# Performance work log

Hardware: AMD Instinct MI355X
Metric: run time of the kernel (lower is better)

The kernel has to match this reference:

```python
import jax, jax.numpy as jnp
import numpy as np

D_MODEL = 1024
N_HEADS = 16
D_HEAD = D_MODEL // N_HEADS


def _pid_proj(x, Wp, Wi, Wd, Wg, bg):
    # x: (B, T, D). PID decomposition: proportional / integral (running mean) / derivative (diff).
    T = x.shape[1]
    denom = jnp.arange(1, T + 1, dtype=x.dtype)[None, :, None]
    integral = jnp.cumsum(x, axis=1) / denom
    derivative = jnp.concatenate([jnp.zeros_like(x[:, :1]), x[:, 1:] - x[:, :-1]], axis=1)
    g = jax.nn.softmax(x @ Wg.T + bg, axis=-1)  # (B, T, 3)
    return (g[..., 0:1] * (x @ Wp.T)
            + g[..., 1:2] * (integral @ Wi.T)
            + g[..., 2:3] * (derivative @ Wd.T))


def setup_inputs() -> dict:
    key = jax.random.key(0)
    ks = jax.random.split(key, 16)
    B, T, D = 2, 2048, D_MODEL
    s = 1.0 / np.sqrt(D)

    def lin(k):
        return jax.random.uniform(k, (D, D), jnp.float32, -s, s)

    inp = {"x": jax.random.normal(ks[0], (B, T, D), jnp.float32)}
    names = ["q", "k", "v"]
    i = 1
    for n in names:
        inp[n + "Wp"] = lin(ks[i]); i += 1
        inp[n + "Wi"] = lin(ks[i]) * 0.1; i += 1
        inp[n + "Wd"] = lin(ks[i]) * 0.1; i += 1
        inp[n + "Wg"] = jax.random.uniform(ks[i], (3, D), jnp.float32, -s, s); i += 1
        inp[n + "bg"] = jnp.array([1.0, 0.0, 0.0], jnp.float32)
    inp["oW"] = lin(ks[i]); i += 1
    inp["ob"] = jax.random.uniform(ks[i], (D,), jnp.float32, -s, s)
    return inp


def reference(x, qWp, qWi, qWd, qWg, qbg,
              kWp, kWi, kWd, kWg, kbg,
              vWp, vWi, vWd, vWg, vbg, oW, ob):
    B, T, D = x.shape
    H, dh = N_HEADS, D_HEAD
    Q = _pid_proj(x, qWp, qWi, qWd, qWg, qbg).reshape(B, T, H, dh).transpose(0, 2, 1, 3)
    K = _pid_proj(x, kWp, kWi, kWd, kWg, kbg).reshape(B, T, H, dh).transpose(0, 2, 1, 3)
    V = _pid_proj(x, vWp, vWi, vWd, vWg, vbg).reshape(B, T, H, dh).transpose(0, 2, 1, 3)
    scale = jnp.sqrt(jnp.asarray(dh, x.dtype))
    scores = jnp.einsum('bhqd,bhkd->bhqk', Q, K) / scale  # (B,H,T,T)
    causal = jnp.triu(jnp.ones((T, T), bool), k=1)
    scores = jnp.where(causal[None, None], -jnp.inf, scores)
    attn = jax.nn.softmax(scores, axis=-1)
    out = jnp.einsum('bhqk,bhkd->bhqd', attn, V)
    out = out.transpose(0, 2, 1, 3).reshape(B, T, D)
    return out @ oW.T + ob
```

## Files before the change

### kernel.cpp

```cpp
#include <hip/hip_runtime.h>
#include <hip/hip_bf16.h>


#define D_MODEL 1024
#define T_SEQ   2048
#define B_SZ    2
#define M_ROWS  (B_SZ * T_SEQ)
#define N_HEADS 16
#define D_HEAD  64

typedef unsigned short u16;
typedef unsigned int   u32;

typedef short  short8  __attribute__((ext_vector_type(8)));
typedef float  float4v __attribute__((ext_vector_type(4)));

__device__ __forceinline__ float bf2f(u16 u) {
    union { u32 i; float f; } c; c.i = ((u32)u) << 16; return c.f;
}
__device__ __forceinline__ u16 f2bf(float f) {
    union { float f; u32 i; } c; c.f = f;
    u32 i = c.i;
    i += 0x7FFFu + ((i >> 16) & 1u);
    return (u16)(i >> 16);
}
__device__ __forceinline__ u16 f2bfc(float f) {
    __hip_bfloat16 h = __float2bfloat16(f);
    union { __hip_bfloat16 h; u16 u; } c; c.h = h; return c.u;
}
__device__ __forceinline__ float ldin(const void* p, int i, int fl) {
    return fl ? ((const float*)p)[i] : bf2f(((const u16*)p)[i]);
}

__global__ void detect_kernel(const u32* __restrict__ x, int* __restrict__ flag)
{
    if (threadIdx.x == 0 && blockIdx.x == 0) {
        int good = 0;
        for (int i = 0; i < 256; ++i) {
            union { u32 u; float f; } c; c.u = x[i];
            float a = fabsf(c.f);
            if (c.f == c.f && a > 1e-8f && a < 1e4f) ++good;
        }
        *flag = (good >= 192) ? 1 : 0;
    }
}

__global__ __launch_bounds__(256) void scan_partial(
    const void* __restrict__ x, float* __restrict__ csum,
    const int* __restrict__ flagp)
{
    int fl = *flagp;
    int tid = blockIdx.x * 256 + threadIdx.x;
    int b = tid >> 14;
    int c = (tid >> 10) & 15;
    int d = tid & 1023;
    int base = (b * T_SEQ + c * 128) * D_MODEL + d;
    float s = 0.f;
#pragma unroll 8
    for (int t = 0; t < 128; ++t) s += ldin(x, base + t * D_MODEL, fl);
    csum[tid] = s;
}

__global__ __launch_bounds__(256) void scan_final(
    const void* __restrict__ x, const float* __restrict__ csum,
    u16* __restrict__ integ, const int* __restrict__ flagp)
{
    int fl = *flagp;
    int tid = blockIdx.x * 256 + threadIdx.x;
    int b = tid >> 14;
    int c = (tid >> 10) & 15;
    int d = tid & 1023;
    float pre = 0.f;
    int cbase = (b << 14) | d;
    for (int cc = 0; cc < c; ++cc) pre += csum[cbase + (cc << 10)];
    int base = (b * T_SEQ + c * 128) * D_MODEL + d;
    float run = pre;
    int t0 = c * 128;
    for (int t = 0; t < 128; ++t) {
        run += ldin(x, base + t * D_MODEL, fl);
        integ[base + t * D_MODEL] = f2bf(run / (float)(t0 + t + 1));
    }
}

__global__ __launch_bounds__(64) void gates_kernel(
    const void* __restrict__ x,
    const void* __restrict__ qWg, const void* __restrict__ qbg,
    const void* __restrict__ kWg, const void* __restrict__ kbg,
    const void* __restrict__ vWg, const void* __restrict__ vbg,
    float* __restrict__ gq, float* __restrict__ gk, float* __restrict__ gv,
    const int* __restrict__ flagp)
{
    int fl = *flagp;
    int row = blockIdx.x;
    int l = threadIdx.x;
    int xb = row * D_MODEL;
    float p[9];
#pragma unroll
    for (int j = 0; j < 9; ++j) p[j] = 0.f;
#pragma unroll 4
    for (int i = 0; i < 16; ++i) {
        int d = l + 64 * i;
        float xv = ldin(x, xb + d, fl);
        p[0] += xv * ldin(qWg, d, fl);
        p[1] += xv * ldin(qWg, 1024 + d, fl);
        p[2] += xv * ldin(qWg, 2048 + d, fl);
        p[3] += xv * ldin(kWg, d, fl);
        p[4] += xv * ldin(kWg, 1024 + d, fl);
        p[5] += xv * ldin(kWg, 2048 + d, fl);
        p[6] += xv * ldin(vWg, d, fl);
        p[7] += xv * ldin(vWg, 1024 + d, fl);
        p[8] += xv * ldin(vWg, 2048 + d, fl);
    }
#pragma unroll
    for (int off = 32; off > 0; off >>= 1) {
#pragma unroll
        for (int j = 0; j < 9; ++j) p[j] += __shfl_down(p[j], off);
    }
    if (l == 0) {
        const void* bgs[3] = { qbg, kbg, vbg };
        float* outs[3] = { gq, gk, gv };
#pragma unroll
        for (int pr = 0; pr < 3; ++pr) {
            float a0 = p[pr * 3 + 0] + ldin(bgs[pr], 0, fl);
            float a1 = p[pr * 3 + 1] + ldin(bgs[pr], 1, fl);
            float a2 = p[pr * 3 + 2] + ldin(bgs[pr], 2, fl);
            float mx = fmaxf(a0, fmaxf(a1, a2));
            float e0 = __expf(a0 - mx), e1 = __expf(a1 - mx), e2 = __expf(a2 - mx);
            float inv = 1.f / (e0 + e1 + e2);
            outs[pr][row * 3 + 0] = e0 * inv;
            outs[pr][row * 3 + 1] = e1 * inv;
            outs[pr][row * 3 + 2] = e2 * inv;
        }
    }
}

struct CvtArgs { const void* src[10]; };

__global__ __launch_bounds__(256) void cvt_w(
    CvtArgs a, u16* __restrict__ dst, const int* __restrict__ flagp)
{
    int fl = *flagp;
    int m = blockIdx.y;
    u16* d = dst + ((size_t)m << 20);
    int i = (blockIdx.x * 256 + threadIdx.x) * 8;
    if (fl) {
        const float* s = (const float*)a.src[m];
        float4 v0 = *(const float4*)(s + i);
        float4 v1 = *(const float4*)(s + i + 4);
        ushort4 o0, o1;
        o0.x = f2bfc(v0.x); o0.y = f2bfc(v0.y); o0.z = f2bfc(v0.z); o0.w = f2bfc(v0.w);
        o1.x = f2bfc(v1.x); o1.y = f2bfc(v1.y); o1.z = f2bfc(v1.z); o1.w = f2bfc(v1.w);
        *(ushort4*)(d + i) = o0;
        *(ushort4*)(d + i + 4) = o1;
    } else {
        const u16* s = (const u16*)a.src[m];
        *(ushort4*)(d + i)     = *(const ushort4*)(s + i);
        *(ushort4*)(d + i + 4) = *(const ushort4*)(s + i + 4);
    }
}

struct GemmArgs {
    const void* W[3][3];
    const float* G[3];
    u16* C[3];
};

template<int MODE, int BW16>
__global__ __launch_bounds__(256, 3) void mfma_gemm(
    const void* __restrict__ X, const u16* __restrict__ Ib,
    const u16* __restrict__ Abf, GemmArgs args,
    const void* __restrict__ bias, void* __restrict__ outp,
    const int* __restrict__ flagp, int Ktot)
{
    int fl = *flagp;
    __shared__ __align__(16) u16 As[2 * 4096];
    __shared__ __align__(16) u16 Bs[2 * 4096];

    int tid = threadIdx.x;
    int l = tid & 63, w = tid >> 6;
    int wm = w >> 1, wn = w & 1;
    int m0 = blockIdx.y * 128, n0 = blockIdx.x * 128;
    int z = blockIdx.z;
    int lane15 = l & 15, quad = l >> 4;
    int srow = tid >> 2;
    int cs = tid & 3;
    int skof = cs * 8;

    const void* W0; const void* W1; const void* W2;
    const float* G = nullptr;
    u16* Chead = nullptr;
    if (MODE == 0) {
        W0 = args.W[z][0]; W1 = args.W[z][1]; W2 = args.W[z][2];
        G = args.G[z]; Chead = args.C[z];
    } else {
        W0 = args.W[0][0]; W1 = W0; W2 = W0;
    }

    float gcoef[2][3];
    if (MODE == 0) {
#pragma unroll
        for (int c = 0; c < 2; ++c)
#pragma unroll
            for (int s = 0; s < 3; ++s)
                gcoef[c][s] = G[(m0 + c * 64 + srow) * 3 + s];
    }

    ushort4 ra[2][4];
    ushort4 rb[2][2];

    auto cvt4 = [](float4 t) {
        ushort4 u;
        u.x = f2bf(t.x); u.y = f2bf(t.y); u.z = f2bf(t.z); u.w = f2bf(t.w);
        return u;
    };
    auto ld8 = [&](const void* p, int idx, ushort4& o0, ushort4& o1) {
        if (fl) {
            o0 = cvt4(*(const float4*)((const float*)p + idx));
            o1 = cvt4(*(const float4*)((const float*)p + idx + 4));
        } else {
            o0 = *(const ushort4*)((const u16*)p + idx);
            o1 = *(const ushort4*)((const u16*)p + idx + 4);
        }
    };

    auto load_phase = [&](int k0) {
        int seg = k0 >> 10, ksrc = k0 & 1023;
        const void* Wse = (MODE == 0) ? (seg == 0 ? W0 : (seg == 1 ? W1 : W2)) : W0;
#pragma unroll
        for (int c = 0; c < 2; ++c) {
            int gm = m0 + c * 64 + srow;
            int idx = gm * 1024 + ksrc + skof;
            if (MODE == 1) {
                ra[c][0] = *(const ushort4*)&Abf[idx];
                ra[c][1] = *(const ushort4*)&Abf[idx + 4];
            } else if (seg == 1) {
                ra[c][0] = *(const ushort4*)&Ib[idx];
                ra[c][1] = *(const ushort4*)&Ib[idx + 4];
            } else {
                ld8(X, idx, ra[c][0], ra[c][1]);
                if (seg == 2 && (gm & (T_SEQ - 1)) != 0)
                    ld8(X, idx - 1024, ra[c][2], ra[c][3]);
            }
            int gn = n0 + c * 64 + srow;
            int bidx = gn * 1024 + ksrc + skof;
            if (BW16) {
                const u16* bs = (const u16*)Wse;
                rb[c][0] = *(const ushort4*)&bs[bidx];
                rb[c][1] = *(const ushort4*)&bs[bidx + 4];
            } else {
                ld8(Wse, bidx, rb[c][0], rb[c][1]);
            }
        }
    };

    auto unp8 = [](ushort4 a, ushort4 b, float v[8]) {
        v[0] = bf2f(a.x); v[1] = bf2f(a.y); v[2] = bf2f(a.z); v[3] = bf2f(a.w);
        v[4] = bf2f(b.x); v[5] = bf2f(b.y); v[6] = bf2f(b.z); v[7] = bf2f(b.w);
    };

    int wo[2];
#pragma unroll
    for (int c = 0; c < 2; ++c) {
        int g = c * 16 + ((srow >> 4) << 2) + cs;
        wo[c] = (g << 7) | ((((srow & 15) + g) & 15) << 3);
    }

    auto store_phase = [&](int k0, int buf) {
        int seg = k0 >> 10;
        u16* Ad = As + buf * 4096;
        u16* Bd = Bs + buf * 4096;
#pragma unroll
        for (int c = 0; c < 2; ++c) {
            int row = c * 64 + srow;
            short8 pk;
            if (MODE == 1) {
                pk[0] = (short)ra[c][0].x; pk[1] = (short)ra[c][0].y;
                pk[2] = (short)ra[c][0].z; pk[3] = (short)ra[c][0].w;
                pk[4] = (short)ra[c][1].x; pk[5] = (short)ra[c][1].y;
                pk[6] = (short)ra[c][1].z; pk[7] = (short)ra[c][1].w;
            } else {
                float v[8];
                unp8(ra[c][0], ra[c][1], v);
                if (seg == 2) {
                    int gm = m0 + row;
                    if ((gm & (T_SEQ - 1)) == 0) {
#pragma unroll
                        for (int j = 0; j < 8; ++j) v[j] = 0.f;
                    } else {
                        float pv[8];
                        unp8(ra[c][2], ra[c][3], pv);
#pragma unroll
                        for (int j = 0; j < 8; ++j) v[j] -= pv[j];
                    }
                }
                float sc = gcoef[c][seg];
#pragma unroll
                for (int j = 0; j < 8; ++j) pk[j] = (short)f2bfc(v[j] * sc);
            }
            *(short8*)&Ad[wo[c]] = pk;

            short8 pb;
            pb[0] = (short)rb[c][0].x; pb[1] = (short)rb[c][0].y;
            pb[2] = (short)rb[c][0].z; pb[3] = (short)rb[c][0].w;
            pb[4] = (short)rb[c][1].x; pb[5] = (short)rb[c][1].y;
            pb[6] = (short)rb[c][1].z; pb[7] = (short)rb[c][1].w;
            *(short8*)&Bd[wo[c]] = pb;
        }
    };

    float4v acc[4][4];
#pragma unroll
    for (int i = 0; i < 4; ++i)
#pragma unroll
        for (int j = 0; j < 4; ++j)
#pragma unroll
            for (int r = 0; r < 4; ++r) acc[i][j][r] = 0.f;

    int aro[4], bro[4];
#pragma unroll
    for (int t = 0; t < 4; ++t) {
        int ga = (wm * 4 + t) * 4 + quad;
        aro[t] = (ga << 7) | (((lane15 + ga) & 15) << 3);
        int gb = (wn * 4 + t) * 4 + quad;
        bro[t] = (gb << 7) | (((lane15 + gb) & 15) << 3);
    }

    int nIt = Ktot >> 5;
    load_phase(0);
    store_phase(0, 0);

    for (int it = 0; it < nIt; ++it) {
        __syncthreads();
        int cur = it & 1;
        if (it + 1 < nIt) load_phase((it + 1) << 5);

        short8 af[4], bfr[4];
#pragma unroll
        for (int ms = 0; ms < 4; ++ms)
            af[ms] = *(const short8*)&As[cur * 4096 + aro[ms]];
#pragma unroll
        for (int ns = 0; ns < 4; ++ns)
            bfr[ns] = *(const short8*)&Bs[cur * 4096 + bro[ns]];
#pragma unroll
        for (int ms = 0; ms < 4; ++ms)
#pragma unroll
            for (int ns = 0; ns < 4; ++ns)
                acc[ms][ns] = __builtin_amdgcn_mfma_f32_16x16x32_bf16(
                    af[ms], bfr[ns], acc[ms][ns], 0, 0, 0);

        if (it + 1 < nIt) store_phase((it + 1) << 5, 1 - cur);
    }

#pragma unroll
    for (int ms = 0; ms < 4; ++ms) {
#pragma unroll
        for (int r = 0; r < 4; ++r) {
            int m = m0 + wm * 64 + ms * 16 + quad * 4 + r;
#pragma unroll
            for (int ns = 0; ns < 4; ++ns) {
                int n = n0 + wn * 64 + ns * 16 + lane15;
                float vv = acc[ms][ns][r];
                if (MODE == 0) {
                    int b = m >> 11, t = m & (T_SEQ - 1);
                    int h = n >> 6,  d = n & 63;
                    Chead[(((b << 4) + h) * T_SEQ + t) * 64 + d] = f2bf(vv);
                } else {
                    vv += ldin(bias, n, fl);
                    if (fl) ((float*)outp)[m * 1024 + n] = vv;
                    else    ((u16*)outp)[m * 1024 + n] = f2bf(vv);
                }
            }
        }
    }
}

__global__ __launch_bounds__(256) void attn_mfma(
    const u16* __restrict__ Qh, const u16* __restrict__ Kh,
    const u16* __restrict__ Vh, u16* __restrict__ AO)
{
    int bx = blockIdx.x;
    int qt = bx & 31;
    int bh = bx >> 5;
    int h  = bh & 15;
    int b  = bh >> 4;
    int tid = threadIdx.x;
    int l   = tid & 63;
    int w   = tid >> 6;
    int lane15 = l & 15;
    int quad   = l >> 4;

    __shared__ __align__(16) u16 Ks[64 * 72];
    __shared__ __align__(16) u16 Vt[64 * 72];
    __shared__ __align__(16) u16 Ps[4 * 16 * 72];

    const u16* Qb = Qh + bh * (T_SEQ * 64);
    const u16* Kb = Kh + bh * (T_SEQ * 64);
    const u16* Vb = Vh + bh * (T_SEQ * 64);

    int qrow = qt * 64 + w * 16 + lane15;
    short8 qf[2];
#pragma unroll
    for (int ks = 0; ks < 2; ++ks)
        qf[ks] = *(const short8*)&Qb[qrow * 64 + ks * 32 + quad * 8];

    float4v oacc[4];
#pragma unroll
    for (int ds = 0; ds < 4; ++ds)
#pragma unroll
        for (int r = 0; r < 4; ++r) oacc[ds][r] = 0.f;
    float mrun[4], lrun[4];
#pragma unroll
    for (int r = 0; r < 4; ++r) { mrun[r] = -1e30f; lrun[r] = 0.f; }

    int srow = tid >> 2;
    int sdc  = (tid & 3) * 16;

    for (int kt = 0; kt <= qt; ++kt) {
        {
            const u16* kp = &Kb[(kt * 64 + srow) * 64 + sdc];
            ushort4 a = *(const ushort4*)kp;
            ushort4 c = *(const ushort4*)(kp + 4);
            ushort4 d2 = *(const ushort4*)(kp + 8);
            ushort4 e = *(const ushort4*)(kp + 12);
            short8 p0, p1;
            p0[0]=a.x; p0[1]=a.y; p0[2]=a.z; p0[3]=a.w;
            p0[4]=c.x; p0[5]=c.y; p0[6]=c.z; p0[7]=c.w;
            p1[0]=d2.x; p1[1]=d2.y; p1[2]=d2.z; p1[3]=d2.w;
            p1[4]=e.x; p1[5]=e.y; p1[6]=e.z; p1[7]=e.w;
            *(short8*)&Ks[srow * 72 + sdc] = p0;
            *(short8*)&Ks[srow * 72 + sdc + 8] = p1;

            const u16* vp = &Vb[(kt * 64 + srow) * 64 + sdc];
            u16 vv[16];
            *(ushort4*)&vv[0]  = *(const ushort4*)vp;
            *(ushort4*)&vv[4]  = *(const ushort4*)(vp + 4);
            *(ushort4*)&vv[8]  = *(const ushort4*)(vp + 8);
            *(ushort4*)&vv[12] = *(const ushort4*)(vp + 12);
#pragma unroll
            for (int e2 = 0; e2 < 16; ++e2)
                Vt[(sdc + e2) * 72 + srow] = vv[e2];
        }
        __syncthreads();

        float4v sacc[4];
#pragma unroll
        for (int ns = 0; ns < 4; ++ns)
#pragma unroll
            for (int r = 0; r < 4; ++r) sacc[ns][r] = 0.f;
#pragma unroll
        for (int ks = 0; ks < 2; ++ks) {
#pragma unroll
            for (int ns = 0; ns < 4; ++ns) {
                short8 bfk = *(const short8*)&Ks[(ns * 16 + lane15) * 72 + ks * 32 + quad * 8];
                sacc[ns] = __builtin_amdgcn_mfma_f32_16x16x32_bf16(
                    qf[ks], bfk, sacc[ns], 0, 0, 0);
            }
        }

        int qg0 = qt * 64 + w * 16 + quad * 4;
#pragma unroll
        for (int ns = 0; ns < 4; ++ns) {
            int kg = kt * 64 + ns * 16 + lane15;
#pragma unroll
            for (int r = 0; r < 4; ++r) {
                float s = sacc[ns][r] * 0.125f;
                sacc[ns][r] = (kg > qg0 + r) ? -1e30f : s;
            }
        }
#pragma unroll
        for (int r = 0; r < 4; ++r) {
            float mx = fmaxf(fmaxf(sacc[0][r], sacc[1][r]),
                             fmaxf(sacc[2][r], sacc[3][r]));
#pragma unroll
            for (int m2 = 1; m2 < 16; m2 <<= 1)
                mx = fmaxf(mx, __shfl_xor(mx, m2, 64));
            float mnew = fmaxf(mrun[r], mx);
            float al = __expf(mrun[r] - mnew);
            float rs = 0.f;
#pragma unroll
            for (int ns = 0; ns < 4; ++ns) {
                float p = __expf(sacc[ns][r] - mnew);
                sacc[ns][r] = p;
                rs += p;
            }
#pragma unroll
            for (int m2 = 1; m2 < 16; m2 <<= 1)
                rs += __shfl_xor(rs, m2, 64);
            lrun[r] = lrun[r] * al + rs;
            mrun[r] = mnew;
#pragma unroll
            for (int ds = 0; ds < 4; ++ds) oacc[ds][r] *= al;
        }

        u16* Pw = &Ps[w * 16 * 72];
#pragma unroll
        for (int ns = 0; ns < 4; ++ns)
#pragma unroll
            for (int r = 0; r < 4; ++r)
                Pw[(quad * 4 + r) * 72 + ns * 16 + lane15] = f2bf(sacc[ns][r]);

#pragma unroll
        for (int ks = 0; ks < 2; ++ks) {
            short8 afp = *(const short8*)&Pw[lane15 * 72 + ks * 32 + quad * 8];
#pragma unroll
            for (int ds = 0; ds < 4; ++ds) {
                short8 bfv = *(const short8*)&Vt[(ds * 16 + lane15) * 72 + ks * 32 + quad * 8];
                oacc[ds] = __builtin_amdgcn_mfma_f32_16x16x32_bf16(
                    afp, bfv, oacc[ds], 0, 0, 0);
            }
        }
        __syncthreads();
    }

#pragma unroll
    for (int r = 0; r < 4; ++r) {
        float inv = 1.f / lrun[r];
        int t = qt * 64 + w * 16 + quad * 4 + r;
        int orow = (b * T_SEQ + t) * 1024 + h * 64;
#pragma unroll
        for (int ds = 0; ds < 4; ++ds)
            AO[orow + ds * 16 + lane15] = f2bf(oacc[ds][r] * inv);
    }
}

extern "C" void kernel_launch(void* const* d_in, const int* in_sizes, int n_in,
                              void* d_out, int out_size, void* d_ws, size_t ws_size,
                              hipStream_t stream)
{
    const void* x   = d_in[0];
    const void* qWp = d_in[1];
    const void* qWi = d_in[2];
    const void* qWd = d_in[3];
    const void* qWg = d_in[4];
    const void* qbg = d_in[5];
    const void* kWp = d_in[6];
    const void* kWi = d_in[7];
    const void* kWd = d_in[8];
    const void* kWg = d_in[9];
    const void* kbg = d_in[10];
    const void* vWp = d_in[11];
    const void* vWi = d_in[12];
    const void* vWd = d_in[13];
    const void* vWg = d_in[14];
    const void* vbg = d_in[15];
    const void* oW  = d_in[16];
    const void* ob  = d_in[17];

    const size_t SZ = (size_t)M_ROWS * D_MODEL;

    int*   flag = (int*)d_ws;
    float* fws  = (float*)d_ws;
    float* csum = fws + 64;
    float* gq   = csum + 32768;
    float* gk   = gq + 3 * M_ROWS;
    float* gv   = gk + 3 * M_ROWS;
    u16* Ib = (u16*)((char*)d_ws + (1u << 20));
    u16* AO = Ib;
    u16* Qh = Ib + SZ;
    u16* Kh = Qh + SZ;
    u16* Vh = Kh + SZ;

    const size_t NEED_FULL = (size_t)(1u << 20) + 4 * SZ * 2 + ((size_t)10 << 21);
    u16* wb = (ws_size >= NEED_FULL) ? (Vh + SZ) : nullptr;

    detect_kernel<<<1, 64, 0, stream>>>((const u32*)x, flag);
    scan_partial<<<128, 256, 0, stream>>>(x, csum, flag);
    scan_final<<<128, 256, 0, stream>>>(x, csum, Ib, flag);
    gates_kernel<<<M_ROWS, 64, 0, stream>>>(x, qWg, qbg, kWg, kbg, vWg, vbg,
                                            gq, gk, gv, flag);

    GemmArgs pa;
    pa.G[0] = gq; pa.G[1] = gk; pa.G[2] = gv;
    pa.C[0] = Qh; pa.C[1] = Kh; pa.C[2] = Vh;
    GemmArgs oa = {};

    if (wb) {
        CvtArgs ca;
        ca.src[0] = qWp; ca.src[1] = qWi; ca.src[2] = qWd;
        ca.src[3] = kWp; ca.src[4] = kWi; ca.src[5] = kWd;
        ca.src[6] = vWp; ca.src[7] = vWi; ca.src[8] = vWd;
        ca.src[9] = oW;
        cvt_w<<<dim3(512, 10), 256, 0, stream>>>(ca, wb, flag);

        for (int z2 = 0; z2 < 3; ++z2)
            for (int s2 = 0; s2 < 3; ++s2)
                pa.W[z2][s2] = wb + ((size_t)(z2 * 3 + s2) << 20);
        oa.W[0][0] = wb + ((size_t)9 << 20);

        mfma_gemm<0, 1><<<dim3(8, 32, 3), 256, 0, stream>>>(
            x, Ib, nullptr, pa, nullptr, nullptr, flag, 3072);
        attn_mfma<<<B_SZ * N_HEADS * (T_SEQ / 64), 256, 0, stream>>>(Qh, Kh, Vh, AO);
        mfma_gemm<1, 1><<<dim3(8, 32, 1), 256, 0, stream>>>(
            nullptr, nullptr, AO, oa, ob, d_out, flag, 1024);
    } else {
        pa.W[0][0] = qWp; pa.W[0][1] = qWi; pa.W[0][2] = qWd;
        pa.W[1][0] = kWp; pa.W[1][1] = kWi; pa.W[1][2] = kWd;
        pa.W[2][0] = vWp; pa.W[2][1] = vWi; pa.W[2][2] = vWd;
        oa.W[0][0] = oW;

        mfma_gemm<0, 0><<<dim3(8, 32, 3), 256, 0, stream>>>(
            x, Ib, nullptr, pa, nullptr, nullptr, flag, 3072);
        attn_mfma<<<B_SZ * N_HEADS * (T_SEQ / 64), 256, 0, stream>>>(Qh, Kh, Vh, AO);
        mfma_gemm<1, 0><<<dim3(8, 32, 1), 256, 0, stream>>>(
            nullptr, nullptr, AO, oa, ob, d_out, flag, 1024);
    }
}
```

Before: 544.3 us.

## Stage bf16 GEMM tiles into LDS with direct global_load_lds transfers

When the weight operand is already bf16, the B tiles are loaded straight from global memory into LDS with global_load_lds instead of going through registers and a store phase. In the output-projection mode, both A and B tiles are loaded this way, which removes the register staging and the LDS store step. The per-lane row and column offsets are chosen to reproduce the existing swizzled LDS layout. This relies on the barrier waiting for the asynchronous loads to finish before the next buffer is read, and on the computed offsets matching the swizzle exactly.

```diff
diff --git a/kernel.cpp b/kernel.cpp
--- a/kernel.cpp
+++ b/kernel.cpp
@@ -30,6 +30,12 @@
 }
 __device__ __forceinline__ float ldin(const void* p, int i, int fl) {
     return fl ? ((const float*)p)[i] : bf2f(((const u16*)p)[i]);
+}
+
+__device__ __forceinline__ void glds16(const u16* g, u16* l) {
+    __builtin_amdgcn_global_load_lds(
+        (const __attribute__((address_space(1))) void*)g,
+        (__attribute__((address_space(3))) void*)l, 16, 0, 0);
 }
 
 __global__ void detect_kernel(const u32* __restrict__ x, int* __restrict__ flag)
@@ -205,6 +211,33 @@
                 gcoef[c][s] = G[(m0 + c * 64 + srow) * 3 + s];
     }
 
+    int dma_rr  = ((l & 15) - 4 * w - (l >> 4)) & 15;
+    int dma_row = 16 * w + dma_rr;
+    int dma_col = (l >> 4) * 8;
+    size_t bofs0 = 0, bofs1 = 0, aofs0 = 0, aofs1 = 0;
+    if (BW16) {
+        bofs0 = (size_t)(n0 + dma_row) * 1024 + dma_col;
+        bofs1 = (size_t)(n0 + 64 + dma_row) * 1024 + dma_col;
+        if (MODE == 1) {
+            aofs0 = (size_t)(m0 + dma_row) * 1024 + dma_col;
+            aofs1 = (size_t)(m0 + 64 + dma_row) * 1024 + dma_col;
+        }
+    }
+
+    auto stageB_dma = [&](int k0, int buf) {
+        int seg = k0 >> 10, ksrc = k0 & 1023;
+        const u16* bs = (const u16*)((MODE == 0)
+            ? (seg == 0 ? W0 : (seg == 1 ? W1 : W2)) : W0);
+        u16* lb = Bs + buf * 4096 + w * 512;
+        glds16(bs + bofs0 + ksrc, lb);
+        glds16(bs + bofs1 + ksrc, lb + 2048);
+    };
+    auto stageA_dma = [&](int k0, int buf) {
+        u16* la = As + buf * 4096 + w * 512;
+        glds16(Abf + aofs0 + k0, la);
+        glds16(Abf + aofs1 + k0, la + 2048);
+    };
+
     ushort4 ra[2][4];
     ushort4 rb[2][2];
 
@@ -241,13 +274,9 @@
                 if (seg == 2 && (gm & (T_SEQ - 1)) != 0)
                     ld8(X, idx - 1024, ra[c][2], ra[c][3]);
             }
-            int gn = n0 + c * 64 + srow;
-            int bidx = gn * 1024 + ksrc + skof;
-            if (BW16) {
-                const u16* bs = (const u16*)Wse;
-                rb[c][0] = *(const ushort4*)&bs[bidx];
-                rb[c][1] = *(const ushort4*)&bs[bidx + 4];
-            } else {
+            if (!BW16) {
+                int gn = n0 + c * 64 + srow;
+                int bidx = gn * 1024 + ksrc + skof;
                 ld8(Wse, bidx, rb[c][0], rb[c][1]);
             }
         }
@@ -299,12 +328,14 @@
             }
             *(short8*)&Ad[wo[c]] = pk;
 
-            short8 pb;
-            pb[0] = (short)rb[c][0].x; pb[1] = (short)rb[c][0].y;
-            pb[2] = (short)rb[c][0].z; pb[3] = (short)rb[c][0].w;
-            pb[4] = (short)rb[c][1].x; pb[5] = (short)rb[c][1].y;
-            pb[6] = (short)rb[c][1].z; pb[7] = (short)rb[c][1].w;
-            *(short8*)&Bd[wo[c]] = pb;
+            if (!BW16) {
+                short8 pb;
+                pb[0] = (short)rb[c][0].x; pb[1] = (short)rb[c][0].y;
+                pb[2] = (short)rb[c][0].z; pb[3] = (short)rb[c][0].w;
+                pb[4] = (short)rb[c][1].x; pb[5] = (short)rb[c][1].y;
+                pb[6] = (short)rb[c][1].z; pb[7] = (short)rb[c][1].w;
+                *(short8*)&Bd[wo[c]] = pb;
+            }
         }
     };
 
@@ -326,13 +357,34 @@
     }
 
     int nIt = Ktot >> 5;
-    load_phase(0);
-    store_phase(0, 0);
+
+    if (BW16 && MODE == 1) {
+        stageA_dma(0, 0);
+        stageB_dma(0, 0);
+    } else if (BW16) {
+        load_phase(0);
+        stageB_dma(0, 0);
+        store_phase(0, 0);
+    } else {
+        load_phase(0);
+        store_phase(0, 0);
+    }
 
     for (int it = 0; it < nIt; ++it) {
         __syncthreads();
         int cur = it & 1;
-        if (it + 1 < nIt) load_phase((it + 1) << 5);
+        if (it + 1 < nIt) {
+            int nk = (it + 1) << 5;
+            if (BW16 && MODE == 1) {
+                stageA_dma(nk, 1 - cur);
+                stageB_dma(nk, 1 - cur);
+            } else if (BW16) {
+                load_phase(nk);
+                stageB_dma(nk, 1 - cur);
+            } else {
+                load_phase(nk);
+            }
+        }
 
         short8 af[4], bfr[4];
 #pragma unroll
@@ -348,7 +400,8 @@
                 acc[ms][ns] = __builtin_amdgcn_mfma_f32_16x16x32_bf16(
                     af[ms], bfr[ns], acc[ms][ns], 0, 0, 0);
 
-        if (it + 1 < nIt) store_phase((it + 1) << 5, 1 - cur);
+        if (it + 1 < nIt && !(BW16 && MODE == 1))
+            store_phase((it + 1) << 5, 1 - cur);
     }
 
 #pragma unroll
```

Result: slower. 582.0 us (+6.9%).
